# Kernel optimization log

Measured on AMD Instinct MI355X. Metric: run time of the kernel, lower is better.

The kernel has to match this reference:

```python
import jax, jax.numpy as jnp
import numpy as np

NH, HD = 4, 16          # num_heads, head_dim (proj_dim = 64)
SCALE = HD ** -0.5
EPS = 1e-5
G = 16                  # GroupNorm groups = min(16, channels)


def _conv1x1(W, b, x):
    # 1x1 conv == channel-mixing matmul: W (out,in), x (B,in,H,W)
    return jnp.einsum('pc,bchw->bphw', W, x) + b[None, :, None, None]


def _attend(Wq, bq, Wk, bk, Wv, bv, Wo, bo, query, context):
    B, C, H, Wd = query.shape
    N = H * Wd
    q = _conv1x1(Wq, bq, query).astype(jnp.float32).reshape(B, NH, HD, N)
    k = _conv1x1(Wk, bk, context).astype(jnp.float32).reshape(B, NH, HD, N)
    v = _conv1x1(Wv, bv, context).astype(jnp.float32).reshape(B, NH, HD, N)
    attn = jax.nn.softmax(jnp.einsum('bhdn,bhdm->bhnm', q, k) * SCALE, axis=-1)
    out = jnp.einsum('bhdm,bhnm->bhdn', v, attn).reshape(B, NH * HD, H, Wd)
    return _conv1x1(Wo, bo, out)


def _gn(x, gamma, beta):
    B, C, H, W = x.shape
    xr = x.reshape(B, G, C // G, H, W)
    m = xr.mean(axis=(2, 3, 4), keepdims=True)
    v = xr.var(axis=(2, 3, 4), keepdims=True)
    xn = ((xr - m) * jax.lax.rsqrt(v + EPS)).reshape(B, C, H, W)
    return xn * gamma[None, :, None, None] + beta[None, :, None, None]


def setup_inputs() -> dict:
    key = jax.random.key(0)
    C, P, Bn, H, W = 256, 64, 2, 64, 64
    ks = iter(jax.random.split(key, 64))
    d = {}
    for m in ['a', 'b', 'c']:
        d[f'feat_{m}'] = jax.random.normal(next(ks), (Bn, C, H, W), jnp.float32)
    for m in ['a', 'b', 'c']:
        d[f'Wq_{m}'] = 0.02 * jax.random.normal(next(ks), (P, C), jnp.float32)
        d[f'bq_{m}'] = jnp.zeros((P,), jnp.float32)
        d[f'Wk_{m}'] = 0.02 * jax.random.normal(next(ks), (P, 2 * C), jnp.float32)
        d[f'bk_{m}'] = jnp.zeros((P,), jnp.float32)
        d[f'Wv_{m}'] = 0.02 * jax.random.normal(next(ks), (P, 2 * C), jnp.float32)
        d[f'bv_{m}'] = jnp.zeros((P,), jnp.float32)
        d[f'Wo_{m}'] = 0.02 * jax.random.normal(next(ks), (C, P), jnp.float32)
        d[f'bo_{m}'] = jnp.zeros((C,), jnp.float32)
        d[f'g_{m}'] = jnp.ones((C,), jnp.float32)
        d[f'be_{m}'] = jnp.zeros((C,), jnp.float32)
    return d


def reference(feat_a, feat_b, feat_c,
              Wq_a, bq_a, Wk_a, bk_a, Wv_a, bv_a, Wo_a, bo_a, g_a, be_a,
              Wq_b, bq_b, Wk_b, bk_b, Wv_b, bv_b, Wo_b, bo_b, g_b, be_b,
              Wq_c, bq_c, Wk_c, bk_c, Wv_c, bv_c, Wo_c, bo_c, g_c, be_c):
    bc = jnp.concatenate([feat_b, feat_c], axis=1)
    a_out = _gn(feat_a + _attend(Wq_a, bq_a, Wk_a, bk_a, Wv_a, bv_a, Wo_a, bo_a, feat_a, bc), g_a, be_a)
    ac = jnp.concatenate([feat_a, feat_c], axis=1)
    b_out = _gn(feat_b + _attend(Wq_b, bq_b, Wk_b, bk_b, Wv_b, bv_b, Wo_b, bo_b, feat_b, ac), g_b, be_b)
    ab = jnp.concatenate([feat_a, feat_b], axis=1)
    c_out = _gn(feat_c + _attend(Wq_c, bq_c, Wk_c, bk_c, Wv_c, bv_c, Wo_c, bo_c, feat_c, ab), g_c, be_c)
    return (a_out, b_out, c_out)
```

## Files before the change

kernel.cpp:

```cpp
#include <hip/hip_runtime.h>

#define B_ 2
#define C_ 256
#define P_ 64
#define N_ 4096
#define EPS_ 1e-5f
#define QSCALE_ 0.3606737602222409f

typedef _Float16 half4 __attribute__((ext_vector_type(4)));
typedef _Float16 half8 __attribute__((ext_vector_type(8)));
typedef float f32x4 __attribute__((ext_vector_type(4)));

static __device__ __forceinline__ float fexp2(float x) {
  return __builtin_bit_cast(float, (int)fmaf(x, 8388608.0f, 1064872512.0f));
}

struct TP {
  const float* feat[3];
  const float* Wq[3]; const float* bq[3];
  const float* Wk[3]; const float* bk[3];
  const float* Wv[3]; const float* bv[3];
  const float* Wo[3]; const float* bo[3];
  const float* gm[3]; const float* bt[3];
  _Float16* q16;
  _Float16* k16;
  _Float16* v16;
  float* stats;
  float* out;
  int ctx0[3]; int ctx1[3];
};

#define PST_ 264
#define VTS_ 88

__global__ __launch_bounds__(256) void proj_fused_kernel(TP P) {
  __shared__ _Float16 bs[64 * PST_];
  const int m = blockIdx.z, b = blockIdx.y;
  const int tid = threadIdx.x;
  const int w = tid >> 6, g = (tid >> 4) & 3, t = tid & 15;
  const bool is_q = blockIdx.x >= 64;
  const int n0 = (is_q ? blockIdx.x - 64 : (int)blockIdx.x) * 64;
  const int sn = tid & 63, scb = (tid >> 6) * 16;

  if (is_q) {
    const float* __restrict__ in = P.feat[m] + (size_t)b * C_ * N_ + n0 + sn;
#pragma unroll
    for (int cc = 0; cc < 4; ++cc) {
      const int c0 = cc * 64 + scb;
      float f[16];
#pragma unroll
      for (int i = 0; i < 16; ++i) f[i] = in[(size_t)(c0 + i) * N_];
      half8 h0, h1;
#pragma unroll
      for (int j = 0; j < 8; ++j) { h0[j] = (_Float16)f[j]; h1[j] = (_Float16)f[8 + j]; }
      *(half8*)(bs + sn * PST_ + c0) = h0;
      *(half8*)(bs + sn * PST_ + c0 + 8) = h1;
    }
    __syncthreads();
    f32x4 a[4] = {{0.f,0.f,0.f,0.f},{0.f,0.f,0.f,0.f},{0.f,0.f,0.f,0.f},{0.f,0.f,0.f,0.f}};
    const float* __restrict__ Wq = P.Wq[m] + (w * 16 + t) * 256;
#pragma unroll
    for (int ks = 0; ks < 8; ++ks) {
      const float4 wa = *(const float4*)(Wq + ks * 32 + g * 8);
      const float4 wb = *(const float4*)(Wq + ks * 32 + g * 8 + 4);
      half8 af;
      af[0] = (_Float16)wa.x; af[1] = (_Float16)wa.y;
      af[2] = (_Float16)wa.z; af[3] = (_Float16)wa.w;
      af[4] = (_Float16)wb.x; af[5] = (_Float16)wb.y;
      af[6] = (_Float16)wb.z; af[7] = (_Float16)wb.w;
#pragma unroll
      for (int i = 0; i < 4; ++i) {
        const half8 bf = *(const half8*)(bs + (i * 16 + t) * PST_ + ks * 32 + g * 8);
        a[i] = __builtin_amdgcn_mfma_f32_16x16x32_f16(af, bf, a[i], 0, 0, 0);
      }
    }
    float bq[4];
#pragma unroll
    for (int r = 0; r < 4; ++r) bq[r] = P.bq[m][w * 16 + g * 4 + r];
    _Float16* qo = P.q16 + ((size_t)(m * 2 + b) * N_) * 64 + w * 16 + g * 4;
#pragma unroll
    for (int i = 0; i < 4; ++i) {
      half4 hq;
#pragma unroll
      for (int r = 0; r < 4; ++r) hq[r] = (_Float16)((a[i][r] + bq[r]) * QSCALE_);
      *(half4*)(qo + (size_t)(n0 + i * 16 + t) * 64) = hq;
    }
  } else {
    f32x4 ka[4] = {{0.f,0.f,0.f,0.f},{0.f,0.f,0.f,0.f},{0.f,0.f,0.f,0.f},{0.f,0.f,0.f,0.f}};
    f32x4 va[4] = {{0.f,0.f,0.f,0.f},{0.f,0.f,0.f,0.f},{0.f,0.f,0.f,0.f},{0.f,0.f,0.f,0.f}};
    const int srcs[2] = {P.ctx0[m], P.ctx1[m]};
    for (int src = 0; src < 2; ++src) {
      const float* __restrict__ in =
          P.feat[srcs[src]] + (size_t)b * C_ * N_ + n0 + sn;
      if (src) __syncthreads();
#pragma unroll
      for (int cc = 0; cc < 4; ++cc) {
        const int c0 = cc * 64 + scb;
        float f[16];
#pragma unroll
        for (int i = 0; i < 16; ++i) f[i] = in[(size_t)(c0 + i) * N_];
        half8 h0, h1;
#pragma unroll
        for (int j = 0; j < 8; ++j) { h0[j] = (_Float16)f[j]; h1[j] = (_Float16)f[8 + j]; }
        *(half8*)(bs + sn * PST_ + c0) = h0;
        *(half8*)(bs + sn * PST_ + c0 + 8) = h1;
      }
      __syncthreads();
      const float* __restrict__ Wk = P.Wk[m] + (w * 16 + t) * 512 + src * 256;
      const float* __restrict__ Wv = P.Wv[m] + (w * 16 + t) * 512 + src * 256;
#pragma unroll
      for (int ks = 0; ks < 8; ++ks) {
        const float4 k0 = *(const float4*)(Wk + ks * 32 + g * 8);
        const float4 k1 = *(const float4*)(Wk + ks * 32 + g * 8 + 4);
        const float4 v0 = *(const float4*)(Wv + ks * 32 + g * 8);
        const float4 v1 = *(const float4*)(Wv + ks * 32 + g * 8 + 4);
        half8 ak, av;
        ak[0] = (_Float16)k0.x; ak[1] = (_Float16)k0.y;
        ak[2] = (_Float16)k0.z; ak[3] = (_Float16)k0.w;
        ak[4] = (_Float16)k1.x; ak[5] = (_Float16)k1.y;
        ak[6] = (_Float16)k1.z; ak[7] = (_Float16)k1.w;
        av[0] = (_Float16)v0.x; av[1] = (_Float16)v0.y;
        av[2] = (_Float16)v0.z; av[3] = (_Float16)v0.w;
        av[4] = (_Float16)v1.x; av[5] = (_Float16)v1.y;
        av[6] = (_Float16)v1.z; av[7] = (_Float16)v1.w;
#pragma unroll
        for (int i = 0; i < 4; ++i) {
          const half8 bf = *(const half8*)(bs + (i * 16 + t) * PST_ + ks * 32 + g * 8);
          ka[i] = __builtin_amdgcn_mfma_f32_16x16x32_f16(ak, bf, ka[i], 0, 0, 0);
          va[i] = __builtin_amdgcn_mfma_f32_16x16x32_f16(av, bf, va[i], 0, 0, 0);
        }
      }
    }
    float bk[4], bv[4];
#pragma unroll
    for (int r = 0; r < 4; ++r) {
      bk[r] = P.bk[m][w * 16 + g * 4 + r];
      bv[r] = P.bv[m][w * 16 + g * 4 + r];
    }
    _Float16* ko = P.k16 + ((size_t)(m * 8 + b * 4 + w) * N_) * 16 + g * 4;
#pragma unroll
    for (int i = 0; i < 4; ++i) {
      half4 hk;
#pragma unroll
      for (int r = 0; r < 4; ++r) hk[r] = (_Float16)(ka[i][r] + bk[r]);
      *(half4*)(ko + (size_t)(n0 + i * 16 + t) * 16) = hk;
    }
    __syncthreads();
#pragma unroll
    for (int i = 0; i < 4; ++i)
#pragma unroll
      for (int r = 0; r < 4; ++r)
        bs[(w * 16 + g * 4 + r) * VTS_ + i * 16 + t] = (_Float16)(va[i][r] + bv[r]);
    __syncthreads();
#pragma unroll
    for (int pass = 0; pass < 2; ++pass) {
      const int row = pass * 32 + (tid >> 3);
      const int hh = row >> 4, dd = row & 15, nb = (tid & 7) * 8;
      const half8 hv = *(const half8*)(bs + row * VTS_ + nb);
      *(half8*)(P.v16 + ((size_t)(m * 8 + b * 4 + hh) * 16 + dd) * N_ + n0 + nb) = hv;
    }
  }
}

__global__ __launch_bounds__(512) void attn_kernel(TP P) {
  const int m = blockIdx.z, bh = blockIdx.y;
  const int tid = threadIdx.x;
  if (m == 0 && bh == 0 && blockIdx.x == 0 && tid < 192) P.stats[tid] = 0.f;
  const int w = tid >> 6, g = (tid >> 4) & 3, t = tid & 15;
  const _Float16* __restrict__ kh = P.k16 + ((size_t)(m * 8 + bh) * N_) * 16;
  const _Float16* __restrict__ vh = P.v16 + ((size_t)(m * 8 + bh) * 16) * N_;
  const int b = bh >> 2, h = bh & 3;
  _Float16* qh = P.q16 + ((size_t)(m * 2 + b) * N_) * 64 + h * 16 + g * 4;

  const int q0 = blockIdx.x * 128 + w * 16;
  const half4 qf = *(const half4*)(qh + (size_t)(q0 + t) * 64);

  __shared__ _Float16 ks[256 * 16];
  __shared__ _Float16 vs[16 * 256];

  const int kr = tid >> 1, kc8 = tid & 1;
  const int vr = tid >> 5, vc = tid & 31;
  const _Float16* kgp = kh + (size_t)kr * 16 + kc8 * 8;
  const _Float16* vgp = vh + (size_t)vr * N_ + vc * 8;
  _Float16* ksp = ks + kr * 16 + ((kc8 ^ (kr & 1)) << 3);
  _Float16* vsp = vs + vr * 256 + ((vc ^ vr) << 3);

  half8 kpre = *(const half8*)kgp;
  half8 vpre = *(const half8*)vgp;

  f32x4 lacc = {0.f, 0.f, 0.f, 0.f};
  f32x4 O0 = {0.f,0.f,0.f,0.f}, O1 = {0.f,0.f,0.f,0.f};

  for (int kv0 = 0; kv0 < N_; kv0 += 256) {
    *(half8*)ksp = kpre;
    *(half8*)vsp = vpre;
    __syncthreads();
    const int nxt = (kv0 + 256 < N_) ? kv0 + 256 : 0;
    kpre = *(const half8*)(kgp + (size_t)nxt * 16);
    vpre = *(const half8*)(vgp + nxt);
#pragma unroll
    for (int hc = 0; hc < 4; ++hc) {
      f32x4 s[4];
#pragma unroll
      for (int i = 0; i < 4; ++i) {
        const int sub = hc * 4 + i;
        const half4 kf = *(const half4*)(ks + (sub * 16 + t) * 16 +
                          (((g >> 1) ^ (t & 1)) << 3) + (g & 1) * 4);
        const f32x4 z = {0.f, 0.f, 0.f, 0.f};
        s[i] = __builtin_amdgcn_mfma_f32_16x16x16f16(kf, qf, z, 0, 0, 0);
      }
      half4 pf[4];
#pragma unroll
      for (int i = 0; i < 4; ++i) {
        const float p0 = fexp2(s[i][0]), p1 = fexp2(s[i][1]);
        const float p2 = fexp2(s[i][2]), p3 = fexp2(s[i][3]);
        lacc[0] += p0; lacc[1] += p1; lacc[2] += p2; lacc[3] += p3;
        pf[i][0] = (_Float16)p0; pf[i][1] = (_Float16)p1;
        pf[i][2] = (_Float16)p2; pf[i][3] = (_Float16)p3;
      }
#pragma unroll
      for (int i = 0; i < 4; ++i) {
        const int c = (hc * 4 + i) * 2 + (g >> 1);
        const half4 vf = *(const half4*)(vs + t * 256 + ((c ^ t) << 3) + (g & 1) * 4);
        if (i & 1) O1 = __builtin_amdgcn_mfma_f32_16x16x16f16(vf, pf[i], O1, 0, 0, 0);
        else       O0 = __builtin_amdgcn_mfma_f32_16x16x16f16(vf, pf[i], O0, 0, 0, 0);
      }
    }
    __syncthreads();
  }
  float l = lacc[0] + lacc[1] + lacc[2] + lacc[3];
  l += __shfl_xor(l, 16);
  l += __shfl_xor(l, 32);
  const float inv = 1.0f / l;
  half4 hv;
#pragma unroll
  for (int r = 0; r < 4; ++r) hv[r] = (_Float16)((O0[r] + O1[r]) * inv);
  *(half4*)(qh + (size_t)(q0 + t) * 64) = hv;
}

#define BS_ 72

__global__ __launch_bounds__(256) void wo_resid_kernel(TP P) {
  __shared__ _Float16 as[64 * BS_];
  const int m = blockIdx.z;
  const int b = blockIdx.y >> 2, cblk = blockIdx.y & 3;
  const int n0 = blockIdx.x * 64;
  const int tid = threadIdx.x;
  const int w = tid >> 6, g = (tid >> 4) & 3, t = tid & 15;
  const int c0 = cblk * 64 + w * 16;
  const _Float16* __restrict__ ao = P.q16 + ((size_t)(m * 2 + b) * N_) * 64;
  const int ar = tid >> 2, ac = (tid & 3) * 16;
  const half8 l0 = *(const half8*)(ao + (size_t)(n0 + ar) * 64 + ac);
  const half8 l1 = *(const half8*)(ao + (size_t)(n0 + ar) * 64 + ac + 8);
  *(half8*)(as + ar * BS_ + ac) = l0;
  *(half8*)(as + ar * BS_ + ac + 8) = l1;
  __syncthreads();
  f32x4 acc[4] = {{0.f,0.f,0.f,0.f},{0.f,0.f,0.f,0.f},{0.f,0.f,0.f,0.f},{0.f,0.f,0.f,0.f}};
  const float* __restrict__ Wo = P.Wo[m] + (c0 + t) * 64;
#pragma unroll
  for (int kst = 0; kst < 2; ++kst) {
    const float4 w0 = *(const float4*)(Wo + kst * 32 + g * 8);
    const float4 w1 = *(const float4*)(Wo + kst * 32 + g * 8 + 4);
    half8 a;
    a[0] = (_Float16)w0.x; a[1] = (_Float16)w0.y;
    a[2] = (_Float16)w0.z; a[3] = (_Float16)w0.w;
    a[4] = (_Float16)w1.x; a[5] = (_Float16)w1.y;
    a[6] = (_Float16)w1.z; a[7] = (_Float16)w1.w;
#pragma unroll
    for (int i = 0; i < 4; ++i) {
      const half8 bf = *(const half8*)(as + (i * 16 + t) * BS_ + kst * 32 + g * 8);
      acc[i] = __builtin_amdgcn_mfma_f32_16x16x32_f16(a, bf, acc[i], 0, 0, 0);
    }
  }
  const float* __restrict__ X = P.feat[m] + (size_t)b * C_ * N_;
  float* outb = P.out + (size_t)m * B_ * C_ * N_ + (size_t)b * C_ * N_;
  float s = 0.f, s2 = 0.f;
#pragma unroll
  for (int i = 0; i < 4; ++i) {
    const int n = n0 + i * 16 + t;
#pragma unroll
    for (int r = 0; r < 4; ++r) {
      const int c = c0 + g * 4 + r;
      const float val = acc[i][r] + X[(size_t)c * N_ + n] + P.bo[m][c];
      outb[(size_t)c * N_ + n] = val;
      s += val;
      s2 += val * val;
    }
  }
#pragma unroll
  for (int off = 1; off < 64; off <<= 1) {
    s += __shfl_xor(s, off);
    s2 += __shfl_xor(s2, off);
  }
  if ((tid & 63) == 0) {
    const int group = cblk * 4 + w;
    float* st = P.stats + ((size_t)(m * 2 + b) * 16 + group) * 2;
    atomicAdd(st, s);
    atomicAdd(st + 1, s2);
  }
}

__global__ __launch_bounds__(256) void gn_final_kernel(TP P) {
  const size_t base = ((size_t)blockIdx.x * 256 + threadIdx.x) * 4;
#pragma unroll
  for (int it = 0; it < 4; ++it) {
    const size_t idx = base + (size_t)it * 1572864;
    const int m = (int)(idx >> 21);
    const int rem = (int)(idx & ((1u << 21) - 1));
    const int b = rem >> 20;
    const int c = (rem >> 12) & 255;
    const float* st = P.stats + ((size_t)(m * 2 + b) * 16 + (c >> 4)) * 2;
    const float mean = st[0] * (1.f / 65536.f);
    const float var = st[1] * (1.f / 65536.f) - mean * mean;
    const float rstd = rsqrtf(var + EPS_);
    const float ga = P.gm[m][c] * rstd, be = P.bt[m][c];
    float4 x = *(float4*)(P.out + idx);
    x.x = (x.x - mean) * ga + be;
    x.y = (x.y - mean) * ga + be;
    x.z = (x.z - mean) * ga + be;
    x.w = (x.w - mean) * ga + be;
    *(float4*)(P.out + idx) = x;
  }
}

extern "C" void kernel_launch(void* const* d_in, const int* in_sizes, int n_in,
                              void* d_out, int out_size, void* d_ws, size_t ws_size,
                              hipStream_t stream) {
  TP P;
  for (int m = 0; m < 3; ++m) {
    P.feat[m] = (const float*)d_in[m];
    const int base = 3 + m * 10;
    P.Wq[m] = (const float*)d_in[base + 0];
    P.bq[m] = (const float*)d_in[base + 1];
    P.Wk[m] = (const float*)d_in[base + 2];
    P.bk[m] = (const float*)d_in[base + 3];
    P.Wv[m] = (const float*)d_in[base + 4];
    P.bv[m] = (const float*)d_in[base + 5];
    P.Wo[m] = (const float*)d_in[base + 6];
    P.bo[m] = (const float*)d_in[base + 7];
    P.gm[m] = (const float*)d_in[base + 8];
    P.bt[m] = (const float*)d_in[base + 9];
  }
  _Float16* ws = (_Float16*)d_ws;
  P.q16 = ws;
  P.k16 = ws + 1572864;
  P.v16 = ws + 3145728;
  P.stats = (float*)(ws + 4718592);
  P.out = (float*)d_out;
  P.ctx0[0] = 1; P.ctx1[0] = 2;
  P.ctx0[1] = 0; P.ctx1[1] = 2;
  P.ctx0[2] = 0; P.ctx1[2] = 1;

  proj_fused_kernel<<<dim3(128, 2, 3), dim3(256), 0, stream>>>(P);
  attn_kernel<<<dim3(32, 8, 3), dim3(512), 0, stream>>>(P);
  wo_resid_kernel<<<dim3(64, 8, 3), dim3(256), 0, stream>>>(P);
  gn_final_kernel<<<dim3(1536), dim3(256), 0, stream>>>(P);
}
```

Before: 279.0 us.

## Split attention KV range across two blocks and merge partials in Wo kernel

The attention kernel now splits the 4096 keys into two halves handled by separate blocks, doubling the grid from 768 to 1536 blocks. Each block writes an unnormalised partial output and its row sum, and the Wo/residual kernel adds the two partials and scales by the inverse combined sum before the MFMA. This targets low occupancy or poor CU utilisation in the attention stage. In exchange it adds extra workspace traffic for two fp16 partial outputs plus the L array, and it changes the K shared-memory layout from XOR swizzle to a padded stride. Adding the unnormalised fp16 partials risks overflow, because the softmax has no max subtraction.

```diff
diff --git a/kernel.cpp b/kernel.cpp
--- a/kernel.cpp
+++ b/kernel.cpp
@@ -25,6 +25,9 @@
   _Float16* q16;
   _Float16* k16;
   _Float16* v16;
+  _Float16* ao0;
+  _Float16* ao1;
+  float* L;
   float* stats;
   float* out;
   int ctx0[3]; int ctx1[3];
@@ -162,27 +165,32 @@
   }
 }
 
+#define KST_ 24
+
 __global__ __launch_bounds__(512) void attn_kernel(TP P) {
   const int m = blockIdx.z, bh = blockIdx.y;
   const int tid = threadIdx.x;
   if (m == 0 && bh == 0 && blockIdx.x == 0 && tid < 192) P.stats[tid] = 0.f;
+  const int kvh = blockIdx.x & 1, qb = blockIdx.x >> 1;
+  const int kvbase = kvh * 2048;
   const int w = tid >> 6, g = (tid >> 4) & 3, t = tid & 15;
   const _Float16* __restrict__ kh = P.k16 + ((size_t)(m * 8 + bh) * N_) * 16;
   const _Float16* __restrict__ vh = P.v16 + ((size_t)(m * 8 + bh) * 16) * N_;
   const int b = bh >> 2, h = bh & 3;
-  _Float16* qh = P.q16 + ((size_t)(m * 2 + b) * N_) * 64 + h * 16 + g * 4;
-
-  const int q0 = blockIdx.x * 128 + w * 16;
+  const _Float16* __restrict__ qh =
+      P.q16 + ((size_t)(m * 2 + b) * N_) * 64 + h * 16 + g * 4;
+
+  const int q0 = qb * 128 + w * 16;
   const half4 qf = *(const half4*)(qh + (size_t)(q0 + t) * 64);
 
-  __shared__ _Float16 ks[256 * 16];
+  __shared__ _Float16 ks[256 * KST_];
   __shared__ _Float16 vs[16 * 256];
 
   const int kr = tid >> 1, kc8 = tid & 1;
   const int vr = tid >> 5, vc = tid & 31;
-  const _Float16* kgp = kh + (size_t)kr * 16 + kc8 * 8;
-  const _Float16* vgp = vh + (size_t)vr * N_ + vc * 8;
-  _Float16* ksp = ks + kr * 16 + ((kc8 ^ (kr & 1)) << 3);
+  const _Float16* kgp = kh + (size_t)(kvbase + kr) * 16 + kc8 * 8;
+  const _Float16* vgp = vh + (size_t)vr * N_ + kvbase + vc * 8;
+  _Float16* ksp = ks + kr * KST_ + kc8 * 8;
   _Float16* vsp = vs + vr * 256 + ((vc ^ vr) << 3);
 
   half8 kpre = *(const half8*)kgp;
@@ -191,11 +199,11 @@
   f32x4 lacc = {0.f, 0.f, 0.f, 0.f};
   f32x4 O0 = {0.f,0.f,0.f,0.f}, O1 = {0.f,0.f,0.f,0.f};
 
-  for (int kv0 = 0; kv0 < N_; kv0 += 256) {
+  for (int c0 = 0; c0 < 2048; c0 += 256) {
     *(half8*)ksp = kpre;
     *(half8*)vsp = vpre;
     __syncthreads();
-    const int nxt = (kv0 + 256 < N_) ? kv0 + 256 : 0;
+    const int nxt = (c0 + 256 < 2048) ? c0 + 256 : 0;
     kpre = *(const half8*)(kgp + (size_t)nxt * 16);
     vpre = *(const half8*)(vgp + nxt);
 #pragma unroll
@@ -204,8 +212,8 @@
 #pragma unroll
       for (int i = 0; i < 4; ++i) {
         const int sub = hc * 4 + i;
-        const half4 kf = *(const half4*)(ks + (sub * 16 + t) * 16 +
-                          (((g >> 1) ^ (t & 1)) << 3) + (g & 1) * 4);
+        const half4 kf = *(const half4*)(ks + (sub * 16 + t) * KST_ +
+                                         (g >> 1) * 8 + (g & 1) * 4);
         const f32x4 z = {0.f, 0.f, 0.f, 0.f};
         s[i] = __builtin_amdgcn_mfma_f32_16x16x16f16(kf, qf, z, 0, 0, 0);
       }
@@ -231,11 +239,14 @@
   float l = lacc[0] + lacc[1] + lacc[2] + lacc[3];
   l += __shfl_xor(l, 16);
   l += __shfl_xor(l, 32);
-  const float inv = 1.0f / l;
+  _Float16* aop = (kvh ? P.ao1 : P.ao0) +
+                  ((size_t)(m * 2 + b) * N_ + q0 + t) * 64 + h * 16 + g * 4;
   half4 hv;
 #pragma unroll
-  for (int r = 0; r < 4; ++r) hv[r] = (_Float16)((O0[r] + O1[r]) * inv);
-  *(half4*)(qh + (size_t)(q0 + t) * 64) = hv;
+  for (int r = 0; r < 4; ++r) hv[r] = (_Float16)(O0[r] + O1[r]);
+  *(half4*)aop = hv;
+  if (g == 0 && (tid & 48) == 0)
+    P.L[((size_t)(kvh * 3 + m) * 8 + bh) * N_ + q0 + t] = l;
 }
 
 #define BS_ 72
@@ -248,13 +259,24 @@
   const int tid = threadIdx.x;
   const int w = tid >> 6, g = (tid >> 4) & 3, t = tid & 15;
   const int c0 = cblk * 64 + w * 16;
-  const _Float16* __restrict__ ao = P.q16 + ((size_t)(m * 2 + b) * N_) * 64;
+  const size_t aob = ((size_t)(m * 2 + b) * N_) * 64;
+  const _Float16* __restrict__ a0p = P.ao0 + aob;
+  const _Float16* __restrict__ a1p = P.ao1 + aob;
   const int ar = tid >> 2, ac = (tid & 3) * 16;
-  const half8 l0 = *(const half8*)(ao + (size_t)(n0 + ar) * 64 + ac);
-  const half8 l1 = *(const half8*)(ao + (size_t)(n0 + ar) * 64 + ac + 8);
-  *(half8*)(as + ar * BS_ + ac) = l0;
-  *(half8*)(as + ar * BS_ + ac + 8) = l1;
+  {
+    const size_t off = (size_t)(n0 + ar) * 64 + ac;
+    half8 s0 = *(const half8*)(a0p + off);
+    half8 s1 = *(const half8*)(a0p + off + 8);
+    const half8 u0 = *(const half8*)(a1p + off);
+    const half8 u1 = *(const half8*)(a1p + off + 8);
+#pragma unroll
+    for (int r = 0; r < 8; ++r) { s0[r] += u0[r]; s1[r] += u1[r]; }
+    *(half8*)(as + ar * BS_ + ac) = s0;
+    *(half8*)(as + ar * BS_ + ac + 8) = s1;
+  }
   __syncthreads();
+  const float* __restrict__ L0 = P.L + ((size_t)m * 8 + b * 4) * N_;
+  const float* __restrict__ L1 = P.L + ((size_t)(3 + m) * 8 + b * 4) * N_;
   f32x4 acc[4] = {{0.f,0.f,0.f,0.f},{0.f,0.f,0.f,0.f},{0.f,0.f,0.f,0.f},{0.f,0.f,0.f,0.f}};
   const float* __restrict__ Wo = P.Wo[m] + (c0 + t) * 64;
 #pragma unroll
@@ -266,9 +288,15 @@
     a[2] = (_Float16)w0.z; a[3] = (_Float16)w0.w;
     a[4] = (_Float16)w1.x; a[5] = (_Float16)w1.y;
     a[6] = (_Float16)w1.z; a[7] = (_Float16)w1.w;
+    const int head = kst * 2 + (g >> 1);
 #pragma unroll
     for (int i = 0; i < 4; ++i) {
-      const half8 bf = *(const half8*)(as + (i * 16 + t) * BS_ + kst * 32 + g * 8);
+      const int n = n0 + i * 16 + t;
+      half8 bf = *(const half8*)(as + (i * 16 + t) * BS_ + kst * 32 + g * 8);
+      const float ls = L0[(size_t)head * N_ + n] + L1[(size_t)head * N_ + n];
+      const _Float16 hs = (_Float16)(1.0f / ls);
+#pragma unroll
+      for (int r = 0; r < 8; ++r) bf[r] *= hs;
       acc[i] = __builtin_amdgcn_mfma_f32_16x16x32_f16(a, bf, acc[i], 0, 0, 0);
     }
   }
@@ -345,14 +373,17 @@
   P.q16 = ws;
   P.k16 = ws + 1572864;
   P.v16 = ws + 3145728;
-  P.stats = (float*)(ws + 4718592);
+  P.ao0 = ws + 4718592;
+  P.ao1 = ws + 6291456;
+  P.L = (float*)(ws + 7864320);
+  P.stats = (float*)(ws + 7864320) + 196608;
   P.out = (float*)d_out;
   P.ctx0[0] = 1; P.ctx1[0] = 2;
   P.ctx0[1] = 0; P.ctx1[1] = 2;
   P.ctx0[2] = 0; P.ctx1[2] = 1;
 
   proj_fused_kernel<<<dim3(128, 2, 3), dim3(256), 0, stream>>>(P);
-  attn_kernel<<<dim3(32, 8, 3), dim3(512), 0, stream>>>(P);
+  attn_kernel<<<dim3(64, 8, 3), dim3(512), 0, stream>>>(P);
   wo_resid_kernel<<<dim3(64, 8, 3), dim3(256), 0, stream>>>(P);
   gn_final_kernel<<<dim3(1536), dim3(256), 0, stream>>>(P);
 }
```

Result: faster. 273.2 us (-2.1%).
